# Kernel optimization log

Measured on AMD Instinct MI355X. Metric: run time of the kernel, lower is better.

The kernel has to match this reference:

```python
import jax, jax.numpy as jnp
import numpy as np

DIM = 384; EXP = 2; INNER = EXP * DIM            # 768
QKV_BS = 4
NH_Q = INNER // QKV_BS                            # 192 headwise-proj heads, head_dim 4
NH_M = QKV_BS                                     # 4 mLSTM heads
DH = INNER // NH_M                                # 192
B = 4; H = 32; W = 32; S = H * W                  # 1024 tokens
K = 3                                             # conv kernel
EPS = 1e-6


def setup_inputs() -> dict:
    key = jax.random.key(0)
    ks = jax.random.split(key, 16)
    def n(k, shape, scale):
        return jax.random.normal(k, shape, dtype=jnp.float32) * scale
    return {
        "x": jax.random.normal(ks[0], (B, S, DIM), dtype=jnp.float32),
        "W_up": n(ks[1], (2 * INNER, DIM), 0.02), "b_up": jnp.zeros((2 * INNER,), jnp.float32),
        "Wq": n(ks[2], (NH_Q, QKV_BS, QKV_BS), 0.1), "bq": jnp.zeros((INNER,), jnp.float32),
        "Wk": n(ks[3], (NH_Q, QKV_BS, QKV_BS), 0.1), "bk": jnp.zeros((INNER,), jnp.float32),
        "Wv": n(ks[4], (NH_Q, QKV_BS, QKV_BS), 0.1), "bv": jnp.zeros((INNER,), jnp.float32),
        "conv_w": n(ks[5], (K, K, 1, INNER), 0.1), "conv_b": jnp.zeros((INNER,), jnp.float32),
        "W_ig": n(ks[6], (NH_M, 3 * INNER), 0.01),
        "b_ig": jax.random.normal(ks[7], (NH_M,), dtype=jnp.float32) * 0.1 - 10.0,
        "W_fg": n(ks[8], (NH_M, 3 * INNER), 0.01),
        "b_fg": jnp.linspace(3.0, 6.0, NH_M, dtype=jnp.float32),
        "norm_w": jnp.ones((INNER,), jnp.float32), "norm_b": jnp.zeros((INNER,), jnp.float32),
        "skip": jnp.ones((INNER,), jnp.float32),
        "W_down": n(ks[9], (DIM, INNER), 0.02), "b_down": jnp.zeros((DIM,), jnp.float32),
    }


def _headwise(x, Wh, b):
    # block-diagonal linear: 192 independent 4x4 blocks
    Bx, Sx, _ = x.shape
    xh = x.reshape(Bx, Sx, NH_Q, QKV_BS)
    y = jnp.einsum('bshd,hod->bsho', xh, Wh)
    return y.reshape(Bx, Sx, INNER) + b


def reference(x, W_up, b_up, Wq, bq, Wk, bk, Wv, bv, conv_w, conv_b,
              W_ig, b_ig, W_fg, b_fg, norm_w, norm_b, skip, W_down, b_down):
    x_inner = x @ W_up.T + b_up                        # (B,S,2*INNER)
    x_m, z = jnp.split(x_inner, 2, axis=-1)
    # depthwise 2d conv over the (H,W) token grid
    img = x_m.reshape(B, H, W, INNER)
    conv = jax.lax.conv_general_dilated(
        img, conv_w, window_strides=(1, 1), padding='SAME',
        dimension_numbers=('NHWC', 'HWIO', 'NHWC'), feature_group_count=INNER)
    conv = (conv + conv_b).reshape(B, S, INNER)
    conv_act = jax.nn.silu(conv)
    q = _headwise(conv_act, Wq, bq)
    k = _headwise(conv_act, Wk, bk)
    v = _headwise(x_m, Wv, bv)
    # ---- mLSTM cell (parallel stabilized form) ----
    gate_in = jnp.concatenate([q, k, v], axis=-1)      # (B,S,3*INNER)
    ig = jnp.einsum('bsf,hf->bhs', gate_in, W_ig) + b_ig[None, :, None]   # (B,NH,S)
    fg = jnp.einsum('bsf,hf->bhs', gate_in, W_fg) + b_fg[None, :, None]
    qh = q.reshape(B, S, NH_M, DH).transpose(0, 2, 1, 3)                  # (B,NH,S,DH)
    kh = k.reshape(B, S, NH_M, DH).transpose(0, 2, 1, 3)
    vh = v.reshape(B, S, NH_M, DH).transpose(0, 2, 1, 3)
    log_f = jax.nn.log_sigmoid(fg)                     # (B,NH,S)
    lfc = jnp.cumsum(log_f, axis=-1)                   # cumulative log forget gates
    dmat = lfc[:, :, :, None] - lfc[:, :, None, :]     # [i,j] = lfc[i]-lfc[j]
    mask = jnp.tril(jnp.ones((S, S), dtype=bool))
    log_fg_mat = jnp.where(mask, dmat, -jnp.inf)
    log_D = log_fg_mat + ig[:, :, None, :]             # add input gate of column j
    max_log_D = jnp.max(log_D, axis=-1, keepdims=True)
    Dm = jnp.exp(log_D - max_log_D)
    qkT = jnp.einsum('bhsd,bhtd->bhst', qh, kh) / jnp.sqrt(jnp.float32(DH))
    C = qkT * Dm
    normalizer = jnp.maximum(jnp.abs(C.sum(-1, keepdims=True)), jnp.exp(-max_log_D))
    Cn = C / (normalizer + EPS)
    h = jnp.einsum('bhst,bhtd->bhsd', Cn, vh)          # (B,NH,S,DH)
    # multi-head layernorm over DH (group_norm with NH groups)
    mean = h.mean(-1, keepdims=True)
    var = h.var(-1, keepdims=True)
    hn = (h - mean) * jax.lax.rsqrt(var + 1e-5)
    hn = hn * norm_w.reshape(NH_M, DH)[None, :, None, :] + norm_b.reshape(NH_M, DH)[None, :, None, :]
    h_tilde = hn.transpose(0, 2, 1, 3).reshape(B, S, INNER)
    # ---- skip, output gating, down projection ----
    h_skip = h_tilde + skip * conv_act
    h_state = h_skip * jax.nn.silu(z)
    return h_state @ W_down.T + b_down
```

## Files before the change

kernel.cpp:

```cpp
#include <hip/hip_runtime.h>
#include <hip/hip_bf16.h>


#define B_     4
#define S_     1024
#define DIM_   384
#define INNER_ 768
#define NHM_   4
#define DH_    192
#define NTOK   (B_*S_)
#define SLOTS_ 40

typedef __attribute__((ext_vector_type(8))) __bf16 bf16x8v;
typedef __attribute__((ext_vector_type(4))) float  f32x4;

static __device__ __forceinline__ f32x4 mfma16(bf16x8v a, bf16x8v b, f32x4 c) {
  return __builtin_amdgcn_mfma_f32_16x16x32_bf16(a, b, c, 0, 0, 0);
}

__global__ __launch_bounds__(256) void cast_all_k(
    const float* __restrict__ x, const float* __restrict__ wup,
    const float* __restrict__ wdn,
    __hip_bfloat16* __restrict__ xb, __hip_bfloat16* __restrict__ wub,
    __hip_bfloat16* __restrict__ wdb)
{
  constexpr int N1 = NTOK * DIM_ / 4;
  constexpr int N2 = N1 + 1536 * DIM_ / 4;
  constexpr int N3 = N2 + DIM_ * INNER_ / 4;
  const int i = blockIdx.x * 256 + threadIdx.x;
  if (i >= N3) return;
  const float* src; __hip_bfloat16* dst; int j;
  if (i < N1)      { src = x;   dst = xb;  j = i; }
  else if (i < N2) { src = wup; dst = wub; j = i - N1; }
  else             { src = wdn; dst = wdb; j = i - N2; }
  const float4 v = *(const float4*)&src[(size_t)j * 4];
  dst[j * 4 + 0] = __float2bfloat16(v.x);
  dst[j * 4 + 1] = __float2bfloat16(v.y);
  dst[j * 4 + 2] = __float2bfloat16(v.z);
  dst[j * 4 + 3] = __float2bfloat16(v.w);
}

template<int KD, bool BIAS>
__global__ __launch_bounds__(256) void gemm_lds_k(
    const __hip_bfloat16* __restrict__ A, int lda,
    const __hip_bfloat16* __restrict__ Bw, int ldb,
    const float* __restrict__ bias, float* __restrict__ C, int ldc)
{
  constexpr int NSTEP = KD / 64;
  __shared__ __hip_bfloat16 Al[2][4096];
  __shared__ __hip_bfloat16 Bl[2][4096];
  const int n0 = blockIdx.x * 64, m0 = blockIdx.y * 64;
  const int kofs = blockIdx.z * KD;
  const int tid = threadIdx.x;
  const int wave = tid >> 6, lane = tid & 63;
  const int lrow = lane & 15, lgrp = lane >> 4;

  const __hip_bfloat16* Ap = A + kofs;
  const __hip_bfloat16* Bp = Bw + kofs;
  float* Cp = C + (size_t)blockIdx.z * NTOK * ldc;

  const int r0 = tid >> 2, g0 = tid & 3;
  bf16x8v areg[2], breg[2];
  auto sload = [&](int k0) {
    areg[0] = *(const bf16x8v*)&Ap[(size_t)(m0 + r0) * lda + k0 + g0 * 8];
    breg[0] = *(const bf16x8v*)&Bp[(size_t)(n0 + r0) * ldb + k0 + g0 * 8];
    areg[1] = *(const bf16x8v*)&Ap[(size_t)(m0 + r0) * lda + k0 + 32 + g0 * 8];
    breg[1] = *(const bf16x8v*)&Bp[(size_t)(n0 + r0) * ldb + k0 + 32 + g0 * 8];
  };
  auto swrite = [&](int buf) {
    *(bf16x8v*)&Al[buf][(size_t)tid * 8]         = areg[0];
    *(bf16x8v*)&Bl[buf][(size_t)tid * 8]         = breg[0];
    *(bf16x8v*)&Al[buf][(size_t)(tid + 256) * 8] = areg[1];
    *(bf16x8v*)&Bl[buf][(size_t)(tid + 256) * 8] = breg[1];
  };

  f32x4 acc[4];
  #pragma unroll
  for (int nt = 0; nt < 4; ++nt) acc[nt] = f32x4{0.f, 0.f, 0.f, 0.f};

  sload(0);
  swrite(0);
  __syncthreads();
  int cur = 0;

  for (int ks = 0; ks < NSTEP; ++ks) {
    const bool nxt = (ks + 1 < NSTEP);
    if (nxt) sload((ks + 1) * 64);
    #pragma unroll
    for (int kk = 0; kk < 2; ++kk) {
      const bf16x8v af = *(const bf16x8v*)
          &Al[cur][(size_t)(kk * 256 + (wave * 16 + lrow) * 4 + lgrp) * 8];
      #pragma unroll
      for (int nt = 0; nt < 4; ++nt) {
        const bf16x8v bf = *(const bf16x8v*)
            &Bl[cur][(size_t)(kk * 256 + (nt * 16 + lrow) * 4 + lgrp) * 8];
        acc[nt] = mfma16(af, bf, acc[nt]);
      }
    }
    if (nxt) swrite(cur ^ 1);
    __syncthreads();
    cur ^= 1;
  }

  #pragma unroll
  for (int nt = 0; nt < 4; ++nt) {
    const int n = n0 + nt * 16 + lrow;
    const float bv = BIAS ? bias[n] : 0.f;
    #pragma unroll
    for (int r = 0; r < 4; ++r) {
      const int m = m0 + wave * 16 + lgrp * 4 + r;
      Cp[(size_t)m * ldc + n] = acc[nt][r] + bv;
    }
  }
}

__global__ __launch_bounds__(256) void gemm_down_red_k(
    const float* __restrict__ pws, const float* __restrict__ bias,
    float* __restrict__ out)
{
  const int i = blockIdx.x * 256 + threadIdx.x;
  if (i >= NTOK * DIM_ / 4) return;
  const int n4 = (i % (DIM_ / 4)) * 4;
  const float4 bv = *(const float4*)&bias[n4];
  float4 s0 = *(const float4*)&pws[(size_t)i * 4];
  const float4 s1 = *(const float4*)&pws[(size_t)NTOK * DIM_ + (size_t)i * 4];
  s0.x += s1.x + bv.x;
  s0.y += s1.y + bv.y;
  s0.z += s1.z + bv.z;
  s0.w += s1.w + bv.w;
  *(float4*)&out[(size_t)i * 4] = s0;
}

__global__ __launch_bounds__(256) void conv_headwise_k(
    const float* __restrict__ xi, const float* __restrict__ cw,
    const float* __restrict__ cb, float* __restrict__ conv_a,
    const float* __restrict__ Wq, const float* __restrict__ bq,
    const float* __restrict__ Wk, const float* __restrict__ bk,
    const float* __restrict__ Wv, const float* __restrict__ bv,
    const float* __restrict__ Wig, const float* __restrict__ big,
    const float* __restrict__ Wfg, const float* __restrict__ bfg,
    __hip_bfloat16* __restrict__ qbf, __hip_bfloat16* __restrict__ kbf,
    __hip_bfloat16* __restrict__ vbf,
    float* __restrict__ ig, float* __restrict__ fg)
{
  __shared__ float cas[INNER_], qs[INNER_], ks[INNER_], vs[INNER_];
  const int t = blockIdx.x;
  const int b = t >> 10, s = t & 1023;
  const int y = s >> 5, x = s & 31;
  const int tb = t - s;
  const int tid = threadIdx.x;

  if (tid < 192) {
    const int c4 = tid * 4;
    float4 acc = *(const float4*)&cb[c4];
    #pragma unroll
    for (int ky = -1; ky <= 1; ++ky) {
      const int yy = y + ky;
      if (yy < 0 || yy > 31) continue;
      #pragma unroll
      for (int kx = -1; kx <= 1; ++kx) {
        const int xx = x + kx;
        if (xx < 0 || xx > 31) continue;
        const float4 v = *(const float4*)&xi[(size_t)(tb + (yy << 5) + xx) * 1536 + c4];
        const float4 w = *(const float4*)&cw[((ky + 1) * 3 + (kx + 1)) * INNER_ + c4];
        acc.x += v.x * w.x; acc.y += v.y * w.y;
        acc.z += v.z * w.z; acc.w += v.w * w.w;
      }
    }
    float4 o;
    o.x = acc.x / (1.f + __expf(-acc.x));
    o.y = acc.y / (1.f + __expf(-acc.y));
    o.z = acc.z / (1.f + __expf(-acc.z));
    o.w = acc.w / (1.f + __expf(-acc.w));
    *(float4*)&cas[c4] = o;
    *(float4*)&conv_a[(size_t)t * INNER_ + c4] = o;
  }
  __syncthreads();

  if (tid < 192) {
    const float4 cav4 = *(const float4*)&cas[tid * 4];
    const float4 xmv4 = *(const float4*)&xi[(size_t)t * 1536 + tid * 4];
    const float cav[4] = {cav4.x, cav4.y, cav4.z, cav4.w};
    const float xmv[4] = {xmv4.x, xmv4.y, xmv4.z, xmv4.w};
    __hip_bfloat16 tq[4], tk[4], tv[4];
    #pragma unroll
    for (int o = 0; o < 4; ++o) {
      const int cidx = tid * 4 + o;
      float q = bq[cidx], k = bk[cidx], v = bv[cidx];
      #pragma unroll
      for (int d = 0; d < 4; ++d) {
        q += cav[d] * Wq[tid * 16 + o * 4 + d];
        k += cav[d] * Wk[tid * 16 + o * 4 + d];
        v += xmv[d] * Wv[tid * 16 + o * 4 + d];
      }
      qs[cidx] = q; ks[cidx] = k; vs[cidx] = v;
      tq[o] = __float2bfloat16(q);
      tk[o] = __float2bfloat16(k);
      tv[o] = __float2bfloat16(v);
    }
    const int cidx0 = tid * 4;
    const int hm = cidx0 / DH_, dd = cidx0 % DH_;
    const size_t o2 = ((size_t)(b * NHM_ + hm) * S_ + s) * DH_ + dd;
    *(uint2*)&qbf[o2] = *(uint2*)tq;
    *(uint2*)&kbf[o2] = *(uint2*)tk;
    *(uint2*)&vbf[o2] = *(uint2*)tv;
  }
  __syncthreads();

  const int g = tid >> 5, l32 = tid & 31;
  const float* Wg = (g < 4) ? Wig : Wfg;
  const int h = g & 3;
  float sum = 0.f;
  #pragma unroll
  for (int i = 0; i < 6; ++i) {
    const int c4 = (l32 + i * 32) * 4;
    const float4 qv = *(const float4*)&qs[c4];
    const float4 kv = *(const float4*)&ks[c4];
    const float4 vv = *(const float4*)&vs[c4];
    const float4 wq = *(const float4*)&Wg[h * 2304 + c4];
    const float4 wk = *(const float4*)&Wg[h * 2304 + 768 + c4];
    const float4 wv = *(const float4*)&Wg[h * 2304 + 1536 + c4];
    sum += qv.x * wq.x + qv.y * wq.y + qv.z * wq.z + qv.w * wq.w;
    sum += kv.x * wk.x + kv.y * wk.y + kv.z * wk.z + kv.w * wk.w;
    sum += vv.x * wv.x + vv.y * wv.y + vv.z * wv.z + vv.w * wv.w;
  }
  #pragma unroll
  for (int m = 16; m >= 1; m >>= 1) sum += __shfl_xor(sum, m);
  if (l32 == 0) {
    if (g < 4) ig[(size_t)(b * NHM_ + h) * S_ + s] = sum + big[h];
    else       fg[(size_t)(b * NHM_ + h) * S_ + s] = sum + bfg[h];
  }
}

__global__ __launch_bounds__(256) void transpose_v_k(
    const __hip_bfloat16* __restrict__ vbf, __hip_bfloat16* __restrict__ vtb)
{
  __shared__ __hip_bfloat16 tile[64][72];
  const int s0 = blockIdx.x * 64, d0 = blockIdx.y * 64, bh = blockIdx.z;
  const int tid = threadIdx.x;
  const int rr = tid >> 3;
  const int cc8 = (tid & 7) * 8;
  #pragma unroll
  for (int it = 0; it < 2; ++it) {
    const int r = rr + it * 32;
    *(bf16x8v*)&tile[r][cc8] =
        *(const bf16x8v*)&vbf[((size_t)bh * S_ + s0 + r) * DH_ + d0 + cc8];
  }
  __syncthreads();
  #pragma unroll
  for (int it = 0; it < 2; ++it) {
    const int r = rr + it * 32;
    bf16x8v tmp;
    #pragma unroll
    for (int e = 0; e < 8; ++e) tmp[e] = *(__bf16*)&tile[cc8 + e][r];
    *(bf16x8v*)&vtb[((size_t)bh * DH_ + d0 + r) * S_ + s0 + cc8] = tmp;
  }
}

__global__ __launch_bounds__(64) void gate_scan_k(
    const float* __restrict__ ig, const float* __restrict__ fg,
    float* __restrict__ lfc, float* __restrict__ aa, float* __restrict__ rm)
{
  const int bh = blockIdx.x;
  const int lane = threadIdx.x;
  const float* fgp = fg + bh * S_;
  const float* igp = ig + bh * S_;
  float v[16];
  float run = 0.f;
  #pragma unroll
  for (int i = 0; i < 16; ++i) {
    const float x = fgp[lane * 16 + i];
    const float lf = fminf(x, 0.f) - log1pf(expf(-fabsf(x)));
    run += lf;
    v[i] = run;
  }
  float inc = run;
  #pragma unroll
  for (int off = 1; off < 64; off <<= 1) {
    const float o = __shfl_up(inc, off);
    if (lane >= off) inc += o;
  }
  const float excl = inc - run;
  float rv[16];
  float rmx = -INFINITY;
  #pragma unroll
  for (int i = 0; i < 16; ++i) {
    const float l = v[i] + excl;
    lfc[bh * S_ + lane * 16 + i] = l;
    const float a = igp[lane * 16 + i] - l;
    aa[bh * S_ + lane * 16 + i] = a;
    rmx = fmaxf(rmx, a);
    rv[i] = rmx;
  }
  float incm = rmx;
  #pragma unroll
  for (int off = 1; off < 64; off <<= 1) {
    const float o = __shfl_up(incm, off);
    if (lane >= off) incm = fmaxf(incm, o);
  }
  float exm = __shfl_up(incm, 1);
  if (lane == 0) exm = -INFINITY;
  #pragma unroll
  for (int i = 0; i < 16; ++i) {
    rm[bh * S_ + lane * 16 + i] = fmaxf(rv[i], exm);
  }
}

__global__ __launch_bounds__(256) void mlstm_part_k(
    const __hip_bfloat16* __restrict__ qbf, const __hip_bfloat16* __restrict__ kbf,
    const __hip_bfloat16* __restrict__ vtb,
    const float* __restrict__ aa, const float* __restrict__ rm,
    float* __restrict__ pacc, float* __restrict__ rsp)
{
  __shared__ __hip_bfloat16 Kl[2][6144];
  __shared__ __hip_bfloat16 Vl[2][6144];
  __shared__ __hip_bfloat16 Pl[4][16][40];
  const int bh = blockIdx.y;
  const int slot = blockIdx.x;
  int t = 0, base = 0;
  #pragma unroll
  for (int s = 0; s < 16; ++s) {
    const int sz = (s >> 2) + 1;
    if (slot >= base + sz) { base += sz; t = s + 1; }
  }
  const int c = slot - base;
  const int jt_lo = c * 8;
  const int jt_hi = min(jt_lo + 8, 2 * t + 2);

  const int wave = threadIdx.x >> 6, lane = threadIdx.x & 63;
  const int lrow = lane & 15, lgrp = lane >> 4;
  const int q0 = t * 64 + wave * 16;
  const __hip_bfloat16* Q  = qbf + (size_t)bh * S_ * DH_;
  const __hip_bfloat16* Kp = kbf + (size_t)bh * S_ * DH_;
  const __hip_bfloat16* VT = vtb + (size_t)bh * DH_ * S_;
  const float* aap = aa + bh * S_;
  const float* rmp = rm + bh * S_;

  bf16x8v qf[6];
  #pragma unroll
  for (int kk = 0; kk < 6; ++kk)
    qf[kk] = *(const bf16x8v*)&Q[(size_t)(q0 + lrow) * DH_ + kk * 32 + lgrp * 8];
  float rmi[4];
  #pragma unroll
  for (int r = 0; r < 4; ++r) rmi[r] = rmp[q0 + lgrp * 4 + r];

  const f32x4 zero4 = {0.f, 0.f, 0.f, 0.f};
  f32x4 hacc[12];
  #pragma unroll
  for (int dd = 0; dd < 12; ++dd) hacc[dd] = zero4;
  float rs[4] = {0.f, 0.f, 0.f, 0.f};
  const float scale = 0.07216878364870323f;
  const int myqmax = q0 + 15;

  bf16x8v kreg[3], vreg[3];
  const int s0_ = wave * 192 + lane;

  auto stage_load = [&](int j0s) {
    #pragma unroll
    for (int i = 0; i < 3; ++i) {
      const int s = s0_ + i * 64;
      const int kk = s >> 7, jr = (s >> 2) & 31, g = s & 3;
      kreg[i] = *(const bf16x8v*)&Kp[(size_t)(j0s + jr) * DH_ + kk * 32 + g * 8];
      const int d = s >> 2;
      vreg[i] = *(const bf16x8v*)&VT[(size_t)d * S_ + j0s + g * 8];
    }
  };
  auto stage_write = [&](int buf) {
    #pragma unroll
    for (int i = 0; i < 3; ++i) {
      const int s = s0_ + i * 64;
      *(bf16x8v*)&Kl[buf][s << 3] = kreg[i];
      *(bf16x8v*)&Vl[buf][s << 3] = vreg[i];
    }
  };

  stage_load(jt_lo * 32);
  stage_write(0);
  __syncthreads();
  int cur = 0;

  for (int jt = jt_lo; jt < jt_hi; ++jt) {
    const int j0 = jt * 32;
    const bool nxt = (jt + 1 < jt_hi);
    if (nxt) stage_load((jt + 1) * 32);
    if (j0 <= myqmax) {
      f32x4 sacc[2];
      sacc[0] = zero4; sacc[1] = zero4;
      #pragma unroll
      for (int jj = 0; jj < 2; ++jj) {
        #pragma unroll
        for (int kk = 0; kk < 6; ++kk) {
          const bf16x8v kf = *(const bf16x8v*)
              &Kl[cur][(kk * 128 + (jj * 16 + lrow) * 4 + lgrp) << 3];
          sacc[jj] = mfma16(qf[kk], kf, sacc[jj]);
        }
      }
      #pragma unroll
      for (int jj = 0; jj < 2; ++jj) {
        const int j = j0 + jj * 16 + lrow;
        const float ajv = aap[j];
        #pragma unroll
        for (int r = 0; r < 4; ++r) {
          const int i_ = q0 + lgrp * 4 + r;
          float cval = 0.f;
          if (j <= i_) cval = sacc[jj][r] * scale * __expf(ajv - rmi[r]);
          rs[r] += cval;
          Pl[wave][lgrp * 4 + r][jj * 16 + lrow] = __float2bfloat16(cval);
        }
      }
      const bf16x8v pf = *(const bf16x8v*)&Pl[wave][lrow][lgrp * 8];
      #pragma unroll
      for (int dd = 0; dd < 12; ++dd) {
        const bf16x8v vf = *(const bf16x8v*)
            &Vl[cur][(dd * 64 + lrow * 4 + lgrp) << 3];
        hacc[dd] = mfma16(pf, vf, hacc[dd]);
      }
    }
    if (nxt) stage_write(cur ^ 1);
    __syncthreads();
    cur ^= 1;
  }

  #pragma unroll
  for (int r = 0; r < 4; ++r) {
    #pragma unroll
    for (int m = 1; m < 16; m <<= 1) rs[r] += __shfl_xor(rs[r], m);
  }
  const size_t pb16 = ((size_t)bh * SLOTS_ + slot) * 16 + wave * 4 + lgrp;
  #pragma unroll
  for (int dd = 0; dd < 12; ++dd) {
    *(f32x4*)&pacc[(pb16 * 12 + dd) * 64 + lrow * 4] = hacc[dd];
  }
  if (lrow == 0) {
    #pragma unroll
    for (int r = 0; r < 4; ++r)
      rsp[((size_t)bh * SLOTS_ + slot) * 64 + wave * 16 + lgrp * 4 + r] = rs[r];
  }
}

__global__ __launch_bounds__(256) void mlstm_red_k(
    const float* __restrict__ pacc, const float* __restrict__ rsp,
    const float* __restrict__ lfc, const float* __restrict__ rm,
    const float* __restrict__ ca, const float* __restrict__ xi,
    const float* __restrict__ nw, const float* __restrict__ nb,
    const float* __restrict__ skip, __hip_bfloat16* __restrict__ hs)
{
  const int t = blockIdx.x, bh = blockIdx.y;
  const int b = bh >> 2, hm = bh & 3;
  int base = 0;
  #pragma unroll
  for (int s = 0; s < 16; ++s) if (s < t) base += (s >> 2) + 1;
  const int nc = (t >> 2) + 1;

  const int wave = threadIdx.x >> 6, lane = threadIdx.x & 63;
  const int lrow = lane & 15, lgrp = lane >> 4;
  const int q0 = t * 64 + wave * 16;
  const float* lfcp = lfc + bh * S_;
  const float* rmp  = rm + bh * S_;

  f32x4 hsum[12];
  #pragma unroll
  for (int dd = 0; dd < 12; ++dd) hsum[dd] = f32x4{0.f, 0.f, 0.f, 0.f};
  float rst[4] = {0.f, 0.f, 0.f, 0.f};

  for (int cc = 0; cc < nc; ++cc) {
    const size_t pb16 = ((size_t)bh * SLOTS_ + base + cc) * 16 + wave * 4 + lgrp;
    #pragma unroll
    for (int dd = 0; dd < 12; ++dd) {
      const f32x4 p = *(const f32x4*)&pacc[(pb16 * 12 + dd) * 64 + lrow * 4];
      hsum[dd] += p;
    }
    #pragma unroll
    for (int r = 0; r < 4; ++r)
      rst[r] += rsp[((size_t)bh * SLOTS_ + base + cc) * 64 + wave * 16 + lgrp * 4 + r];
  }

  #pragma unroll
  for (int r = 0; r < 4; ++r) {
    const int i_ = q0 + lgrp * 4 + r;
    const int tok = b * S_ + i_;
    const float mld = lfcp[i_] + rmp[i_];
    const float nrm = fmaxf(fabsf(rst[r]), __expf(-mld)) + 1e-6f;
    float hv[12];
    float sum = 0.f, sq = 0.f;
    #pragma unroll
    for (int dd = 0; dd < 12; ++dd) {
      const float x = hsum[dd][r] / nrm;
      hv[dd] = x; sum += x; sq += x * x;
    }
    #pragma unroll
    for (int m = 1; m < 16; m <<= 1) {
      sum += __shfl_xor(sum, m);
      sq  += __shfl_xor(sq, m);
    }
    const float mean = sum * (1.f / 192.f);
    const float var  = sq * (1.f / 192.f) - mean * mean;
    const float rstd = rsqrtf(var + 1e-5f);
    #pragma unroll
    for (int dd = 0; dd < 12; ++dd) {
      const int cidx = hm * DH_ + dd * 16 + lrow;
      const float hn = (hv[dd] - mean) * rstd * nw[cidx] + nb[cidx];
      const float cav = ca[(size_t)tok * INNER_ + cidx];
      const float zz  = xi[(size_t)tok * 1536 + 768 + cidx];
      const float hsv = (hn + skip[cidx] * cav) * (zz / (1.f + __expf(-zz)));
      hs[(size_t)tok * INNER_ + cidx] = __float2bfloat16(hsv);
    }
  }
}

extern "C" void kernel_launch(void* const* d_in, const int* in_sizes, int n_in,
                              void* d_out, int out_size, void* d_ws, size_t ws_size,
                              hipStream_t stream) {
  const float* x      = (const float*)d_in[0];
  const float* W_up   = (const float*)d_in[1];
  const float* b_up   = (const float*)d_in[2];
  const float* Wq     = (const float*)d_in[3];
  const float* bq     = (const float*)d_in[4];
  const float* Wk     = (const float*)d_in[5];
  const float* bk     = (const float*)d_in[6];
  const float* Wv     = (const float*)d_in[7];
  const float* bv     = (const float*)d_in[8];
  const float* conv_w = (const float*)d_in[9];
  const float* conv_b = (const float*)d_in[10];
  const float* W_ig   = (const float*)d_in[11];
  const float* b_ig   = (const float*)d_in[12];
  const float* W_fg   = (const float*)d_in[13];
  const float* b_fg   = (const float*)d_in[14];
  const float* norm_w = (const float*)d_in[15];
  const float* norm_b = (const float*)d_in[16];
  const float* skip   = (const float*)d_in[17];
  const float* W_down = (const float*)d_in[18];
  const float* b_down = (const float*)d_in[19];
  float* out = (float*)d_out;

  char* ws = (char*)d_ws;
  constexpr size_t OFF_XI  = 0;
  constexpr size_t OFF_CA  = OFF_XI + (size_t)NTOK * 1536 * 4;
  constexpr size_t OFF_QBF = OFF_CA + (size_t)NTOK * INNER_ * 4;
  constexpr size_t OFF_KBF = OFF_QBF + (size_t)16 * S_ * DH_ * 2;
  constexpr size_t OFF_VBF = OFF_KBF + (size_t)16 * S_ * DH_ * 2;
  constexpr size_t OFF_IG  = OFF_VBF + (size_t)16 * S_ * DH_ * 2;
  constexpr size_t OFF_FG  = OFF_IG + (size_t)16 * S_ * 4;
  constexpr size_t OFF_LFC = OFF_FG + (size_t)16 * S_ * 4;
  constexpr size_t OFF_AA  = OFF_LFC + (size_t)16 * S_ * 4;
  constexpr size_t OFF_RM  = OFF_AA + (size_t)16 * S_ * 4;
  constexpr size_t OFF_HS  = OFF_RM + (size_t)16 * S_ * 4;
  constexpr size_t OFF_XB  = OFF_HS + (size_t)NTOK * INNER_ * 4;
  constexpr size_t OFF_WUB = OFF_XB + (size_t)NTOK * DIM_ * 2;
  constexpr size_t OFF_PAC = OFF_WUB + (size_t)1536 * DIM_ * 2;
  constexpr size_t OFF_RSP = OFF_PAC + (size_t)16 * SLOTS_ * 64 * 192 * 4;
  constexpr size_t OFF_WDB = OFF_RSP + (size_t)16 * SLOTS_ * 64 * 4;
  constexpr size_t OFF_VTB = OFF_WDB + (size_t)DIM_ * INNER_ * 2;

  float* x_inner = (float*)(ws + OFF_XI);
  float* conv_a  = (float*)(ws + OFF_CA);
  __hip_bfloat16* qbf = (__hip_bfloat16*)(ws + OFF_QBF);
  __hip_bfloat16* kbf = (__hip_bfloat16*)(ws + OFF_KBF);
  __hip_bfloat16* vbf = (__hip_bfloat16*)(ws + OFF_VBF);
  float* ig  = (float*)(ws + OFF_IG);
  float* fg  = (float*)(ws + OFF_FG);
  float* lfc = (float*)(ws + OFF_LFC);
  float* aav = (float*)(ws + OFF_AA);
  float* rmv = (float*)(ws + OFF_RM);
  __hip_bfloat16* hsb = (__hip_bfloat16*)(ws + OFF_HS);
  __hip_bfloat16* xb  = (__hip_bfloat16*)(ws + OFF_XB);
  __hip_bfloat16* wub = (__hip_bfloat16*)(ws + OFF_WUB);
  float* pacc = (float*)(ws + OFF_PAC);
  float* rsp  = (float*)(ws + OFF_RSP);
  __hip_bfloat16* wdb = (__hip_bfloat16*)(ws + OFF_WDB);
  __hip_bfloat16* vtb = (__hip_bfloat16*)(ws + OFF_VTB);
  float* pws = pacc;

  {
    constexpr int N3 = NTOK * DIM_ / 4 + 1536 * DIM_ / 4 + DIM_ * INNER_ / 4;
    cast_all_k<<<(N3 + 255) / 256, 256, 0, stream>>>(x, W_up, W_down, xb, wub, wdb);
  }
  gemm_lds_k<DIM_, true><<<dim3(24, 64, 1), 256, 0, stream>>>(
      xb, DIM_, wub, DIM_, b_up, x_inner, 1536);
  conv_headwise_k<<<NTOK, 256, 0, stream>>>(
      x_inner, conv_w, conv_b, conv_a,
      Wq, bq, Wk, bk, Wv, bv, W_ig, b_ig, W_fg, b_fg,
      qbf, kbf, vbf, ig, fg);
  transpose_v_k<<<dim3(16, 3, 16), 256, 0, stream>>>(vbf, vtb);
  gate_scan_k<<<16, 64, 0, stream>>>(ig, fg, lfc, aav, rmv);
  mlstm_part_k<<<dim3(SLOTS_, 16), 256, 0, stream>>>(qbf, kbf, vtb, aav, rmv, pacc, rsp);
  mlstm_red_k<<<dim3(16, 16), 256, 0, stream>>>(
      pacc, rsp, lfc, rmv, conv_a, x_inner, norm_w, norm_b, skip, hsb);
  gemm_lds_k<DIM_, false><<<dim3(6, 64, 2), 256, 0, stream>>>(
      hsb, INNER_, wdb, INNER_, nullptr, pws, DIM_);
  gemm_down_red_k<<<(NTOK * DIM_ / 4 + 255) / 256, 256, 0, stream>>>(pws, b_down, out);
}
```

Before: 128.7 us.

## Fuse SiLU(z) into up-GEMM epilogue, store bf16 intermediates, merge aux kernels

```diff
diff --git a/kernel.cpp b/kernel.cpp
--- a/kernel.cpp
+++ b/kernel.cpp
@@ -40,11 +40,85 @@
   dst[j * 4 + 3] = __float2bfloat16(v.w);
 }
 
-template<int KD, bool BIAS>
+__global__ __launch_bounds__(256) void gemm_up_lds_k(
+    const __hip_bfloat16* __restrict__ A,
+    const __hip_bfloat16* __restrict__ Bw,
+    const float* __restrict__ bias, float* __restrict__ xm,
+    __hip_bfloat16* __restrict__ gz)
+{
+  constexpr int NSTEP = DIM_ / 64;
+  __shared__ __hip_bfloat16 Al[2][4096];
+  __shared__ __hip_bfloat16 Bl[2][4096];
+  const int n0 = blockIdx.x * 64, m0 = blockIdx.y * 64;
+  const int tid = threadIdx.x;
+  const int wave = tid >> 6, lane = tid & 63;
+  const int lrow = lane & 15, lgrp = lane >> 4;
+
+  const int r0 = tid >> 2, g0 = tid & 3;
+  bf16x8v areg[2], breg[2];
+  auto sload = [&](int k0) {
+    areg[0] = *(const bf16x8v*)&A[(size_t)(m0 + r0) * DIM_ + k0 + g0 * 8];
+    breg[0] = *(const bf16x8v*)&Bw[(size_t)(n0 + r0) * DIM_ + k0 + g0 * 8];
+    areg[1] = *(const bf16x8v*)&A[(size_t)(m0 + r0) * DIM_ + k0 + 32 + g0 * 8];
+    breg[1] = *(const bf16x8v*)&Bw[(size_t)(n0 + r0) * DIM_ + k0 + 32 + g0 * 8];
+  };
+  auto swrite = [&](int buf) {
+    *(bf16x8v*)&Al[buf][(size_t)tid * 8]         = areg[0];
+    *(bf16x8v*)&Bl[buf][(size_t)tid * 8]         = breg[0];
+    *(bf16x8v*)&Al[buf][(size_t)(tid + 256) * 8] = areg[1];
+    *(bf16x8v*)&Bl[buf][(size_t)(tid + 256) * 8] = breg[1];
+  };
+
+  f32x4 acc[4];
+  #pragma unroll
+  for (int nt = 0; nt < 4; ++nt) acc[nt] = f32x4{0.f, 0.f, 0.f, 0.f};
+
+  sload(0); swrite(0);
+  __syncthreads();
+  int cur = 0;
+  for (int ks = 0; ks < NSTEP; ++ks) {
+    const bool nxt = (ks + 1 < NSTEP);
+    if (nxt) sload((ks + 1) * 64);
+    #pragma unroll
+    for (int kk = 0; kk < 2; ++kk) {
+      const bf16x8v af = *(const bf16x8v*)
+          &Al[cur][(size_t)(kk * 256 + (wave * 16 + lrow) * 4 + lgrp) * 8];
+      #pragma unroll
+      for (int nt = 0; nt < 4; ++nt) {
+        const bf16x8v bf = *(const bf16x8v*)
+            &Bl[cur][(size_t)(kk * 256 + (nt * 16 + lrow) * 4 + lgrp) * 8];
+        acc[nt] = mfma16(af, bf, acc[nt]);
+      }
+    }
+    if (nxt) swrite(cur ^ 1);
+    __syncthreads();
+    cur ^= 1;
+  }
+
+  const bool zside = (n0 >= INNER_);
+  #pragma unroll
+  for (int nt = 0; nt < 4; ++nt) {
+    const int n = n0 + nt * 16 + lrow;
+    const float bv = bias[n];
+    #pragma unroll
+    for (int r = 0; r < 4; ++r) {
+      const int m = m0 + wave * 16 + lgrp * 4 + r;
+      const float v = acc[nt][r] + bv;
+      if (!zside) {
+        xm[(size_t)m * INNER_ + n] = v;
+      } else {
+        gz[(size_t)m * INNER_ + (n - INNER_)] =
+            __float2bfloat16(v / (1.f + __expf(-v)));
+      }
+    }
+  }
+}
+
+template<int KD>
 __global__ __launch_bounds__(256) void gemm_lds_k(
     const __hip_bfloat16* __restrict__ A, int lda,
     const __hip_bfloat16* __restrict__ Bw, int ldb,
-    const float* __restrict__ bias, float* __restrict__ C, int ldc)
+    float* __restrict__ C, int ldc)
 {
   constexpr int NSTEP = KD / 64;
   __shared__ __hip_bfloat16 Al[2][4096];
@@ -78,11 +152,9 @@
   #pragma unroll
   for (int nt = 0; nt < 4; ++nt) acc[nt] = f32x4{0.f, 0.f, 0.f, 0.f};
 
-  sload(0);
-  swrite(0);
+  sload(0); swrite(0);
   __syncthreads();
   int cur = 0;
-
   for (int ks = 0; ks < NSTEP; ++ks) {
     const bool nxt = (ks + 1 < NSTEP);
     if (nxt) sload((ks + 1) * 64);
@@ -105,11 +177,10 @@
   #pragma unroll
   for (int nt = 0; nt < 4; ++nt) {
     const int n = n0 + nt * 16 + lrow;
-    const float bv = BIAS ? bias[n] : 0.f;
     #pragma unroll
     for (int r = 0; r < 4; ++r) {
       const int m = m0 + wave * 16 + lgrp * 4 + r;
-      Cp[(size_t)m * ldc + n] = acc[nt][r] + bv;
+      Cp[(size_t)m * ldc + n] = acc[nt][r];
     }
   }
 }
@@ -132,8 +203,8 @@
 }
 
 __global__ __launch_bounds__(256) void conv_headwise_k(
-    const float* __restrict__ xi, const float* __restrict__ cw,
-    const float* __restrict__ cb, float* __restrict__ conv_a,
+    const float* __restrict__ xm, const float* __restrict__ cw,
+    const float* __restrict__ cb, __hip_bfloat16* __restrict__ cab,
     const float* __restrict__ Wq, const float* __restrict__ bq,
     const float* __restrict__ Wk, const float* __restrict__ bk,
     const float* __restrict__ Wv, const float* __restrict__ bv,
@@ -161,7 +232,7 @@
       for (int kx = -1; kx <= 1; ++kx) {
         const int xx = x + kx;
         if (xx < 0 || xx > 31) continue;
-        const float4 v = *(const float4*)&xi[(size_t)(tb + (yy << 5) + xx) * 1536 + c4];
+        const float4 v = *(const float4*)&xm[(size_t)(tb + (yy << 5) + xx) * INNER_ + c4];
         const float4 w = *(const float4*)&cw[((ky + 1) * 3 + (kx + 1)) * INNER_ + c4];
         acc.x += v.x * w.x; acc.y += v.y * w.y;
         acc.z += v.z * w.z; acc.w += v.w * w.w;
@@ -173,13 +244,15 @@
     o.z = acc.z / (1.f + __expf(-acc.z));
     o.w = acc.w / (1.f + __expf(-acc.w));
     *(float4*)&cas[c4] = o;
-    *(float4*)&conv_a[(size_t)t * INNER_ + c4] = o;
+    __hip_bfloat16 tc[4] = {__float2bfloat16(o.x), __float2bfloat16(o.y),
+                            __float2bfloat16(o.z), __float2bfloat16(o.w)};
+    *(uint2*)&cab[(size_t)t * INNER_ + c4] = *(uint2*)tc;
   }
   __syncthreads();
 
   if (tid < 192) {
     const float4 cav4 = *(const float4*)&cas[tid * 4];
-    const float4 xmv4 = *(const float4*)&xi[(size_t)t * 1536 + tid * 4];
+    const float4 xmv4 = *(const float4*)&xm[(size_t)t * INNER_ + tid * 4];
     const float cav[4] = {cav4.x, cav4.y, cav4.z, cav4.w};
     const float xmv[4] = {xmv4.x, xmv4.y, xmv4.z, xmv4.w};
     __hip_bfloat16 tq[4], tk[4], tv[4];
@@ -232,36 +305,39 @@
   }
 }
 
-__global__ __launch_bounds__(256) void transpose_v_k(
-    const __hip_bfloat16* __restrict__ vbf, __hip_bfloat16* __restrict__ vtb)
-{
-  __shared__ __hip_bfloat16 tile[64][72];
-  const int s0 = blockIdx.x * 64, d0 = blockIdx.y * 64, bh = blockIdx.z;
-  const int tid = threadIdx.x;
-  const int rr = tid >> 3;
-  const int cc8 = (tid & 7) * 8;
-  #pragma unroll
-  for (int it = 0; it < 2; ++it) {
-    const int r = rr + it * 32;
-    *(bf16x8v*)&tile[r][cc8] =
-        *(const bf16x8v*)&vbf[((size_t)bh * S_ + s0 + r) * DH_ + d0 + cc8];
-  }
-  __syncthreads();
-  #pragma unroll
-  for (int it = 0; it < 2; ++it) {
-    const int r = rr + it * 32;
-    bf16x8v tmp;
-    #pragma unroll
-    for (int e = 0; e < 8; ++e) tmp[e] = *(__bf16*)&tile[cc8 + e][r];
-    *(bf16x8v*)&vtb[((size_t)bh * DH_ + d0 + r) * S_ + s0 + cc8] = tmp;
-  }
-}
-
-__global__ __launch_bounds__(64) void gate_scan_k(
+__global__ __launch_bounds__(256) void aux_k(
+    const __hip_bfloat16* __restrict__ vbf, __hip_bfloat16* __restrict__ vtb,
     const float* __restrict__ ig, const float* __restrict__ fg,
     float* __restrict__ lfc, float* __restrict__ aa, float* __restrict__ rm)
 {
-  const int bh = blockIdx.x;
+  const int blk = blockIdx.x;
+  if (blk < 768) {
+    __shared__ __hip_bfloat16 tile[64][72];
+    const int s0 = (blk & 15) * 64;
+    const int d0 = ((blk >> 4) % 3) * 64;
+    const int bh = blk / 48;
+    const int tid = threadIdx.x;
+    const int rr = tid >> 3;
+    const int cc8 = (tid & 7) * 8;
+    #pragma unroll
+    for (int it = 0; it < 2; ++it) {
+      const int r = rr + it * 32;
+      *(bf16x8v*)&tile[r][cc8] =
+          *(const bf16x8v*)&vbf[((size_t)bh * S_ + s0 + r) * DH_ + d0 + cc8];
+    }
+    __syncthreads();
+    #pragma unroll
+    for (int it = 0; it < 2; ++it) {
+      const int r = rr + it * 32;
+      bf16x8v tmp;
+      #pragma unroll
+      for (int e = 0; e < 8; ++e) tmp[e] = *(__bf16*)&tile[cc8 + e][r];
+      *(bf16x8v*)&vtb[((size_t)bh * DH_ + d0 + r) * S_ + s0 + cc8] = tmp;
+    }
+    return;
+  }
+  if (threadIdx.x >= 64) return;
+  const int bh = blk - 768;
   const int lane = threadIdx.x;
   const float* fgp = fg + bh * S_;
   const float* igp = ig + bh * S_;
@@ -269,8 +345,8 @@
   float run = 0.f;
   #pragma unroll
   for (int i = 0; i < 16; ++i) {
-    const float x = fgp[lane * 16 + i];
-    const float lf = fminf(x, 0.f) - log1pf(expf(-fabsf(x)));
+    const float xv = fgp[lane * 16 + i];
+    const float lf = fminf(xv, 0.f) - log1pf(expf(-fabsf(xv)));
     run += lf;
     v[i] = run;
   }
@@ -315,8 +391,8 @@
   __shared__ __hip_bfloat16 Kl[2][6144];
   __shared__ __hip_bfloat16 Vl[2][6144];
   __shared__ __hip_bfloat16 Pl[4][16][40];
-  const int bh = blockIdx.y;
-  const int slot = blockIdx.x;
+  const int bh = blockIdx.x;
+  const int slot = blockIdx.y;
   int t = 0, base = 0;
   #pragma unroll
   for (int s = 0; s < 16; ++s) {
@@ -441,7 +517,7 @@
 __global__ __launch_bounds__(256) void mlstm_red_k(
     const float* __restrict__ pacc, const float* __restrict__ rsp,
     const float* __restrict__ lfc, const float* __restrict__ rm,
-    const float* __restrict__ ca, const float* __restrict__ xi,
+    const __hip_bfloat16* __restrict__ cab, const __hip_bfloat16* __restrict__ gz,
     const float* __restrict__ nw, const float* __restrict__ nb,
     const float* __restrict__ skip, __hip_bfloat16* __restrict__ hs)
 {
@@ -500,9 +576,9 @@
     for (int dd = 0; dd < 12; ++dd) {
       const int cidx = hm * DH_ + dd * 16 + lrow;
       const float hn = (hv[dd] - mean) * rstd * nw[cidx] + nb[cidx];
-      const float cav = ca[(size_t)tok * INNER_ + cidx];
-      const float zz  = xi[(size_t)tok * 1536 + 768 + cidx];
-      const float hsv = (hn + skip[cidx] * cav) * (zz / (1.f + __expf(-zz)));
+      const float cav = __bfloat162float(cab[(size_t)tok * INNER_ + cidx]);
+      const float gzv = __bfloat162float(gz[(size_t)tok * INNER_ + cidx]);
+      const float hsv = (hn + skip[cidx] * cav) * gzv;
       hs[(size_t)tok * INNER_ + cidx] = __float2bfloat16(hsv);
     }
   }
@@ -534,9 +610,10 @@
   float* out = (float*)d_out;
 
   char* ws = (char*)d_ws;
-  constexpr size_t OFF_XI  = 0;
-  constexpr size_t OFF_CA  = OFF_XI + (size_t)NTOK * 1536 * 4;
-  constexpr size_t OFF_QBF = OFF_CA + (size_t)NTOK * INNER_ * 4;
+  constexpr size_t OFF_XM  = 0;
+  constexpr size_t OFF_GZ  = OFF_XM + (size_t)NTOK * INNER_ * 4;
+  constexpr size_t OFF_CA  = OFF_GZ + (size_t)NTOK * INNER_ * 2;
+  constexpr size_t OFF_QBF = OFF_CA + (size_t)NTOK * INNER_ * 2;
   constexpr size_t OFF_KBF = OFF_QBF + (size_t)16 * S_ * DH_ * 2;
   constexpr size_t OFF_VBF = OFF_KBF + (size_t)16 * S_ * DH_ * 2;
   constexpr size_t OFF_IG  = OFF_VBF + (size_t)16 * S_ * DH_ * 2;
@@ -545,15 +622,16 @@
   constexpr size_t OFF_AA  = OFF_LFC + (size_t)16 * S_ * 4;
   constexpr size_t OFF_RM  = OFF_AA + (size_t)16 * S_ * 4;
   constexpr size_t OFF_HS  = OFF_RM + (size_t)16 * S_ * 4;
-  constexpr size_t OFF_XB  = OFF_HS + (size_t)NTOK * INNER_ * 4;
+  constexpr size_t OFF_XB  = OFF_HS + (size_t)NTOK * INNER_ * 2;
   constexpr size_t OFF_WUB = OFF_XB + (size_t)NTOK * DIM_ * 2;
-  constexpr size_t OFF_PAC = OFF_WUB + (size_t)1536 * DIM_ * 2;
+  constexpr size_t OFF_WDB = OFF_WUB + (size_t)1536 * DIM_ * 2;
+  constexpr size_t OFF_VTB = OFF_WDB + (size_t)DIM_ * INNER_ * 2;
+  constexpr size_t OFF_PAC = OFF_VTB + (size_t)16 * DH_ * S_ * 2;
   constexpr size_t OFF_RSP = OFF_PAC + (size_t)16 * SLOTS_ * 64 * 192 * 4;
-  constexpr size_t OFF_WDB = OFF_RSP + (size_t)16 * SLOTS_ * 64 * 4;
-  constexpr size_t OFF_VTB = OFF_WDB + (size_t)DIM_ * INNER_ * 2;
-
-  float* x_inner = (float*)(ws + OFF_XI);
-  float* conv_a  = (float*)(ws + OFF_CA);
+
+  float* xm  = (float*)(ws + OFF_XM);
+  __hip_bfloat16* gz  = (__hip_bfloat16*)(ws + OFF_GZ);
+  __hip_bfloat16* cab = (__hip_bfloat16*)(ws + OFF_CA);
   __hip_bfloat16* qbf = (__hip_bfloat16*)(ws + OFF_QBF);
   __hip_bfloat16* kbf = (__hip_bfloat16*)(ws + OFF_KBF);
   __hip_bfloat16* vbf = (__hip_bfloat16*)(ws + OFF_VBF);
@@ -565,28 +643,26 @@
   __hip_bfloat16* hsb = (__hip_bfloat16*)(ws + OFF_HS);
   __hip_bfloat16* xb  = (__hip_bfloat16*)(ws + OFF_XB);
   __hip_bfloat16* wub = (__hip_bfloat16*)(ws + OFF_WUB);
+  __hip_bfloat16* wdb = (__hip_bfloat16*)(ws + OFF_WDB);
+  __hip_bfloat16* vtb = (__hip_bfloat16*)(ws + OFF_VTB);
   float* pacc = (float*)(ws + OFF_PAC);
   float* rsp  = (float*)(ws + OFF_RSP);
-  __hip_bfloat16* wdb = (__hip_bfloat16*)(ws + OFF_WDB);
-  __hip_bfloat16* vtb = (__hip_bfloat16*)(ws + OFF_VTB);
-  float* pws = pacc;
+  float* pws  = pacc;
 
   {
     constexpr int N3 = NTOK * DIM_ / 4 + 1536 * DIM_ / 4 + DIM_ * INNER_ / 4;
     cast_all_k<<<(N3 + 255) / 256, 256, 0, stream>>>(x, W_up, W_down, xb, wub, wdb);
   }
-  gemm_lds_k<DIM_, true><<<dim3(24, 64, 1), 256, 0, stream>>>(
-      xb, DIM_, wub, DIM_, b_up, x_inner, 1536);
+  gemm_up_lds_k<<<dim3(24, 64), 256, 0, stream>>>(xb, wub, b_up, xm, gz);
   conv_headwise_k<<<NTOK, 256, 0, stream>>>(
-      x_inner, conv_w, conv_b, conv_a,
+      xm, conv_w, conv_b, cab,
       Wq, bq, Wk, bk, Wv, bv, W_ig, b_ig, W_fg, b_fg,
       qbf, kbf, vbf, ig, fg);
-  transpose_v_k<<<dim3(16, 3, 16), 256, 0, stream>>>(vbf, vtb);
-  gate_scan_k<<<16, 64, 0, stream>>>(ig, fg, lfc, aav, rmv);
-  mlstm_part_k<<<dim3(SLOTS_, 16), 256, 0, stream>>>(qbf, kbf, vtb, aav, rmv, pacc, rsp);
+  aux_k<<<784, 256, 0, stream>>>(vbf, vtb, ig, fg, lfc, aav, rmv);
+  mlstm_part_k<<<dim3(16, SLOTS_), 256, 0, stream>>>(qbf, kbf, vtb, aav, rmv, pacc, rsp);
   mlstm_red_k<<<dim3(16, 16), 256, 0, stream>>>(
-      pacc, rsp, lfc, rmv, conv_a, x_inner, norm_w, norm_b, skip, hsb);
-  gemm_lds_k<DIM_, false><<<dim3(6, 64, 2), 256, 0, stream>>>(
-      hsb, INNER_, wdb, INNER_, nullptr, pws, DIM_);
+      pacc, rsp, lfc, rmv, cab, gz, norm_w, norm_b, skip, hsb);
+  gemm_lds_k<DIM_><<<dim3(6, 64, 2), 256, 0, stream>>>(
+      hsb, INNER_, wdb, INNER_, pws, DIM_);
   gemm_down_red_k<<<(NTOK * DIM_ / 4 + 255) / 256, 256, 0, stream>>>(pws, b_down, out);
 }
```

Result: faster. 119.6 us (-7.1%).
